# Performance work log

Measured on AMD Instinct MI355X. Metric: run time of the kernel, lower is better.

## Reference

```python
import jax, jax.numpy as jnp
import numpy as np

N_CLASSES = 256
PER_CLASS = 128
N_SUPPORT = 5
N_QUERY = PER_CLASS - N_SUPPORT  # 123
N_VIEW = 2
D = 384
N = N_CLASSES * PER_CLASS  # 32768


def setup_inputs() -> dict:
    key = jax.random.key(0)
    k1, k2 = jax.random.split(key, 2)
    reps = jax.random.normal(k1, (N, N_VIEW, D), dtype=jnp.float32)
    # block-sorted labels: class c occupies rows [c*PER_CLASS, (c+1)*PER_CLASS)
    labels = (jnp.arange(N, dtype=jnp.int32) // PER_CLASS).astype(jnp.int32)
    return {"reps": reps, "labels": labels}


def reference(reps, labels):
    # labels are block-sorted per class, so the original's
    # labels.eq(c).nonzero()[:n_support] / [n_support:] gathers are static reshapes.
    reps_r = reps.reshape(N_CLASSES, PER_CLASS, N_VIEW, D)
    # class-mean prototypes over the support set: [C, V, D]
    prototypes = reps_r[:, :N_SUPPORT].mean(axis=1)
    # query samples: [C*N_QUERY, V, D]
    queries = reps_r[:, N_SUPPORT:].reshape(N_CLASSES * N_QUERY, N_VIEW, D)

    x2 = jnp.sum(queries * queries, axis=-1)            # [n, V]
    y2 = jnp.sum(prototypes * prototypes, axis=-1)      # [m, V]
    xy = jnp.einsum('nvd,mvd->nmv', queries, prototypes)  # [n, m, V]
    dists = x2[:, None, :] + y2[None, :, :] - 2.0 * xy

    # log_softmax over the prototype (class) axis
    log_p_y = jax.nn.log_softmax(-dists, axis=1)
    log_p_y = log_p_y.reshape(N_CLASSES, N_QUERY, N_CLASSES, N_VIEW)

    # gather the true-class log-prob for each query / view
    cls = jnp.arange(N_CLASSES)
    correct = log_p_y[cls, :, cls, :]  # [C, N_QUERY, V]
    loss = -correct.mean()
    return loss
```

## Files before the change

kernel.cpp:

```cpp
#include <hip/hip_runtime.h>
#include <hip/hip_bf16.h>
#include <math.h>

#define NCLS 256
#define PER_CLASS 128
#define NSUP 5
#define NQRY 123
#define NVIEW 2
#define DD 384
#define NQ_TOT (NCLS * NQRY)
#define BM 128
#define BK 32
#define NKT (DD / BK)
#define PS 32
#define NBUF 3

typedef __attribute__((ext_vector_type(8))) short short8;
typedef __attribute__((ext_vector_type(4))) float floatx4;

union FragU { uint4 u; short8 s; };
union PkU { __hip_bfloat162 b2; unsigned int u; };

__device__ __forceinline__ unsigned int cvt2bf(float lo, float hi) {
    PkU p;
    p.b2 = __float22bfloat162_rn(make_float2(lo, hi));
    return p.u;
}

__device__ __forceinline__ void gll16(const ushort* g, ushort* l) {
    __builtin_amdgcn_global_load_lds(
        (const __attribute__((address_space(1))) unsigned int*)g,
        (__attribute__((address_space(3))) unsigned int*)l, 16, 0, 0);
}

#define BARRIER() asm volatile("s_waitcnt lgkmcnt(0)\n\ts_barrier" ::: "memory")
#define WAITVM(n) asm volatile("s_waitcnt vmcnt(" #n ")" ::: "memory")

__global__ __launch_bounds__(384) void proto_kernel(const float* __restrict__ reps,
                                                    ushort* __restrict__ pbf,
                                                    float* __restrict__ y2,
                                                    float* __restrict__ out) {
    __shared__ float wp[6];
    const int b = blockIdx.x;
    const int c = b & 255, v = b >> 8;
    const int d = threadIdx.x;
    if (b == 0 && d == 0) out[0] = 0.f;
    const float* p = reps + ((size_t)(c * PER_CLASS) * NVIEW + v) * DD + d;
    float s = 0.f;
#pragma unroll
    for (int k = 0; k < NSUP; ++k) s += p[(size_t)k * NVIEW * DD];
    s *= 0.2f;
    __hip_bfloat16 h = __float2bfloat16(s);
    pbf[(size_t)b * DD + d] = *reinterpret_cast<ushort*>(&h);
    float q = s * s;
#pragma unroll
    for (int o = 1; o < 64; o <<= 1) q += __shfl_xor(q, o);
    if ((d & 63) == 0) wp[d >> 6] = q;
    __syncthreads();
    if (d == 0) y2[b] = wp[0] + wp[1] + wp[2] + wp[3] + wp[4] + wp[5];
}

__global__ __launch_bounds__(256, 2) void main_kernel(const float* __restrict__ reps,
                                                      const ushort* __restrict__ pbf,
                                                      const float* __restrict__ y2g,
                                                      float* __restrict__ out) {
    __shared__ ushort p_lds[NBUF][NCLS * PS];
    __shared__ float pmx[BM][2];
    __shared__ float pse[BM][2];
    __shared__ float wred[8];

    const int t = threadIdx.x;
    const int v = blockIdx.y;
    const int q0 = blockIdx.x * BM;
    const int wave = t >> 6;
    const int lane = t & 63;
    const int col = lane & 15;
    const int quad = lane >> 4;
    const int wm = wave >> 1;
    const int wn = wave & 1;

    const ushort* psrc = pbf + (size_t)(v * NCLS + wave * 64 + (lane >> 2)) * DD
                             + (((lane & 3) ^ ((lane >> 3) & 3)) << 3);

    const int sP = (col >> 1) & 3;
    const int pbase = (wn * 128 + col) * PS + ((quad ^ sP) << 3);

    const float* qb[4];
#pragma unroll
    for (int mt = 0; mt < 4; ++mt) {
        const int nq = q0 + wm * 64 + mt * 16 + col;
        qb[mt] = reps +
            (size_t)((nq / NQRY) * PER_CLASS + NSUP + (nq % NQRY)) * (NVIEW * DD) +
            v * DD + quad * 8;
    }

    floatx4 acc[4][8];
#pragma unroll
    for (int mt = 0; mt < 4; ++mt)
#pragma unroll
        for (int nt = 0; nt < 8; ++nt) acc[mt][nt] = (floatx4)0.f;

    float4 qv[4][2];

#define LOADQ(kt)                                                                  \
    do {                                                                           \
        _Pragma("unroll") for (int mt = 0; mt < 4; ++mt) {                         \
            qv[mt][0] = *(const float4*)(qb[mt] + (kt) * BK);                      \
            qv[mt][1] = *(const float4*)(qb[mt] + (kt) * BK + 4);                  \
        }                                                                          \
    } while (0)

#define GLLP(kt, b)                                                                \
    do {                                                                           \
        _Pragma("unroll") for (int i = 0; i < 4; ++i)                              \
            gll16(psrc + i * (16 * DD) + (kt) * BK,                                \
                  &p_lds[b][wave * 2048 + i * 512]);                               \
    } while (0)

#define COMPUTE(b)                                                                 \
    do {                                                                           \
        short8 af[4];                                                              \
        _Pragma("unroll") for (int mt = 0; mt < 4; ++mt) {                         \
            FragU f;                                                               \
            f.u.x = cvt2bf(qv[mt][0].x, qv[mt][0].y);                              \
            f.u.y = cvt2bf(qv[mt][0].z, qv[mt][0].w);                              \
            f.u.z = cvt2bf(qv[mt][1].x, qv[mt][1].y);                              \
            f.u.w = cvt2bf(qv[mt][1].z, qv[mt][1].w);                              \
            af[mt] = f.s;                                                          \
        }                                                                          \
        _Pragma("unroll") for (int nt = 0; nt < 8; ++nt) {                         \
            FragU bb;                                                              \
            bb.u = *(const uint4*)&p_lds[b][pbase + nt * 16 * PS];                 \
            _Pragma("unroll") for (int mt = 0; mt < 4; ++mt)                       \
                acc[mt][nt] = __builtin_amdgcn_mfma_f32_16x16x32_bf16(af[mt], bb.s, acc[mt][nt], 0, 0, 0); \
        }                                                                          \
    } while (0)

    GLLP(0, 0);
    GLLP(1, 1);
    WAITVM(4);
    BARRIER();

#pragma unroll
    for (int kt = 0; kt < NKT; ++kt) {
        if (kt < NKT - 2) GLLP(kt + 2, (kt + 2) % NBUF);
        LOADQ(kt);
        if (kt < NKT - 2) {
            WAITVM(12);
        } else {
            WAITVM(0);
        }
        COMPUTE(kt % NBUF);
        if (kt < NKT - 1) BARRIER();
    }

    float y2c[8];
#pragma unroll
    for (int nt = 0; nt < 8; ++nt) y2c[nt] = y2g[v * NCLS + wn * 128 + nt * 16 + col];

    float corr = 0.f;
#pragma unroll
    for (int mt = 0; mt < 4; ++mt) {
#pragma unroll
        for (int r = 0; r < 4; ++r) {
            const int qloc = wm * 64 + mt * 16 + quad * 4 + r;
            const int n = q0 + qloc;
            const int cn = n / NQRY;
            float s[8];
            float mx = -1e30f;
#pragma unroll
            for (int nt = 0; nt < 8; ++nt) {
                s[nt] = 2.f * acc[mt][nt][r] - y2c[nt];
                mx = fmaxf(mx, s[nt]);
                if (cn == wn * 128 + nt * 16 + col) corr += s[nt];
            }
#pragma unroll
            for (int o = 1; o < 16; o <<= 1) mx = fmaxf(mx, __shfl_xor(mx, o));
            float e = 0.f;
#pragma unroll
            for (int nt = 0; nt < 8; ++nt) e += __expf(s[nt] - mx);
#pragma unroll
            for (int o = 1; o < 16; o <<= 1) e += __shfl_xor(e, o);
            if (col == 0) { pmx[qloc][wn] = mx; pse[qloc][wn] = e; }
        }
    }
#pragma unroll
    for (int o = 1; o < 64; o <<= 1) corr += __shfl_xor(corr, o);
    if (lane == 0) wred[wave] = corr;
    __syncthreads();

    float lval = 0.f;
    if (t < BM) {
        float m0 = pmx[t][0], m1 = pmx[t][1];
        float M = fmaxf(m0, m1);
        float E = pse[t][0] * __expf(m0 - M) + pse[t][1] * __expf(m1 - M);
        lval = M + __logf(E);
    }
#pragma unroll
    for (int o = 1; o < 64; o <<= 1) lval += __shfl_xor(lval, o);
    if (lane == 0) wred[4 + wave] = lval;
    __syncthreads();

    if (t == 0) {
        float tot = (wred[4] + wred[5] + wred[6] + wred[7]) -
                    (wred[0] + wred[1] + wred[2] + wred[3]);
        atomicAdd(out, tot * (1.f / (float)(NQ_TOT * NVIEW)));
    }
}

extern "C" void kernel_launch(void* const* d_in, const int* in_sizes, int n_in,
                              void* d_out, int out_size, void* d_ws, size_t ws_size,
                              hipStream_t stream) {
    const float* reps = (const float*)d_in[0];
    float* ws = (float*)d_ws;
    ushort* pbf = (ushort*)ws;
    float* y2 = (float*)(pbf + NVIEW * NCLS * DD);
    float* out = (float*)d_out;

    proto_kernel<<<dim3(NVIEW * NCLS), dim3(DD), 0, stream>>>(reps, pbf, y2, out);
    main_kernel<<<dim3(NQ_TOT / BM, NVIEW), dim3(256), 0, stream>>>(reps, pbf, y2, out);
}
```

Before: 174.3 us.

## Split class axis across blocks with resident prototype LDS and combine kernel

Partitions the 256 prototypes into four 64-class slices handled by separate blocks, each loading its whole bf16 prototype slice into LDS once and streaming queries through a three-deep register prefetch ring. Per-slice partial max and sum-exp are written to global memory and a new combine kernel performs the final log-sum-exp and reduction. This removes per-k-step barriers and LDS buffer rotation and increases block count, but each query row is now read four times from global memory and an extra launch plus intermediate traffic is added.

```diff
diff --git a/kernel.cpp b/kernel.cpp
--- a/kernel.cpp
+++ b/kernel.cpp
@@ -9,11 +9,11 @@
 #define NVIEW 2
 #define DD 384
 #define NQ_TOT (NCLS * NQRY)
-#define BM 128
+#define QB 256
+#define CQ 64
 #define BK 32
 #define NKT (DD / BK)
-#define PS 32
-#define NBUF 3
+#define INV_CNT (1.f / (float)(NQ_TOT * NVIEW))
 
 typedef __attribute__((ext_vector_type(8))) short short8;
 typedef __attribute__((ext_vector_type(4))) float floatx4;
@@ -39,12 +39,13 @@
 __global__ __launch_bounds__(384) void proto_kernel(const float* __restrict__ reps,
                                                     ushort* __restrict__ pbf,
                                                     float* __restrict__ y2,
+                                                    float* __restrict__ wsc,
                                                     float* __restrict__ out) {
     __shared__ float wp[6];
     const int b = blockIdx.x;
     const int c = b & 255, v = b >> 8;
     const int d = threadIdx.x;
-    if (b == 0 && d == 0) out[0] = 0.f;
+    if (b == 0 && d == 0) { out[0] = 0.f; wsc[0] = 0.f; }
     const float* p = reps + ((size_t)(c * PER_CLASS) * NVIEW + v) * DD + d;
     float s = 0.f;
 #pragma unroll
@@ -60,151 +61,165 @@
     if (d == 0) y2[b] = wp[0] + wp[1] + wp[2] + wp[3] + wp[4] + wp[5];
 }
 
-__global__ __launch_bounds__(256, 2) void main_kernel(const float* __restrict__ reps,
-                                                      const ushort* __restrict__ pbf,
-                                                      const float* __restrict__ y2g,
-                                                      float* __restrict__ out) {
-    __shared__ ushort p_lds[NBUF][NCLS * PS];
-    __shared__ float pmx[BM][2];
-    __shared__ float pse[BM][2];
-    __shared__ float wred[8];
+__global__ __launch_bounds__(512) void main_kernel(const float* __restrict__ reps,
+                                                   const ushort* __restrict__ pbf,
+                                                   const float* __restrict__ y2g,
+                                                   float* __restrict__ pmax_g,
+                                                   float* __restrict__ pse_g,
+                                                   float* __restrict__ wsc) {
+    __shared__ ushort p_lds[NKT * CQ * 32];
 
     const int t = threadIdx.x;
     const int v = blockIdx.y;
-    const int q0 = blockIdx.x * BM;
+    const int zq = blockIdx.z;
+    const int q0 = blockIdx.x * QB;
     const int wave = t >> 6;
     const int lane = t & 63;
     const int col = lane & 15;
     const int quad = lane >> 4;
-    const int wm = wave >> 1;
-    const int wn = wave & 1;
-
-    const ushort* psrc = pbf + (size_t)(v * NCLS + wave * 64 + (lane >> 2)) * DD
-                             + (((lane & 3) ^ ((lane >> 3) & 3)) << 3);
-
-    const int sP = (col >> 1) & 3;
-    const int pbase = (wn * 128 + col) * PS + ((quad ^ sP) << 3);
-
-    const float* qb[4];
-#pragma unroll
-    for (int mt = 0; mt < 4; ++mt) {
-        const int nq = q0 + wm * 64 + mt * 16 + col;
+
+#pragma unroll
+    for (int i = 0; i < 6; ++i) {
+        const int g = wave * 6 + i;
+        const int slab = g >> 2;
+        const int sub = g & 3;
+        const ushort* src = pbf +
+            (size_t)(v * NCLS + zq * CQ + sub * 16 + (lane >> 2)) * DD +
+            slab * BK + (lane & 3) * 8;
+        gll16(src, &p_lds[slab * 2048 + sub * 512]);
+    }
+
+    const float* qb[2];
+#pragma unroll
+    for (int mt = 0; mt < 2; ++mt) {
+        const int nq = q0 + wave * 32 + mt * 16 + col;
         qb[mt] = reps +
             (size_t)((nq / NQRY) * PER_CLASS + NSUP + (nq % NQRY)) * (NVIEW * DD) +
             v * DD + quad * 8;
     }
 
-    floatx4 acc[4][8];
-#pragma unroll
-    for (int mt = 0; mt < 4; ++mt)
-#pragma unroll
-        for (int nt = 0; nt < 8; ++nt) acc[mt][nt] = (floatx4)0.f;
-
-    float4 qv[4][2];
-
-#define LOADQ(kt)                                                                  \
+    floatx4 acc[2][4];
+#pragma unroll
+    for (int mt = 0; mt < 2; ++mt)
+#pragma unroll
+        for (int nt = 0; nt < 4; ++nt) acc[mt][nt] = (floatx4)0.f;
+
+    float4 qv[3][2][2];
+
+#define LOADQ(kt, b)                                                               \
     do {                                                                           \
-        _Pragma("unroll") for (int mt = 0; mt < 4; ++mt) {                         \
-            qv[mt][0] = *(const float4*)(qb[mt] + (kt) * BK);                      \
-            qv[mt][1] = *(const float4*)(qb[mt] + (kt) * BK + 4);                  \
+        _Pragma("unroll") for (int mt = 0; mt < 2; ++mt) {                         \
+            qv[b][mt][0] = *(const float4*)(qb[mt] + (kt) * BK);                   \
+            qv[b][mt][1] = *(const float4*)(qb[mt] + (kt) * BK + 4);               \
         }                                                                          \
     } while (0)
 
-#define GLLP(kt, b)                                                                \
-    do {                                                                           \
-        _Pragma("unroll") for (int i = 0; i < 4; ++i)                              \
-            gll16(psrc + i * (16 * DD) + (kt) * BK,                                \
-                  &p_lds[b][wave * 2048 + i * 512]);                               \
-    } while (0)
-
-#define COMPUTE(b)                                                                 \
-    do {                                                                           \
-        short8 af[4];                                                              \
-        _Pragma("unroll") for (int mt = 0; mt < 4; ++mt) {                         \
-            FragU f;                                                               \
-            f.u.x = cvt2bf(qv[mt][0].x, qv[mt][0].y);                              \
-            f.u.y = cvt2bf(qv[mt][0].z, qv[mt][0].w);                              \
-            f.u.z = cvt2bf(qv[mt][1].x, qv[mt][1].y);                              \
-            f.u.w = cvt2bf(qv[mt][1].z, qv[mt][1].w);                              \
-            af[mt] = f.s;                                                          \
-        }                                                                          \
-        _Pragma("unroll") for (int nt = 0; nt < 8; ++nt) {                         \
-            FragU bb;                                                              \
-            bb.u = *(const uint4*)&p_lds[b][pbase + nt * 16 * PS];                 \
-            _Pragma("unroll") for (int mt = 0; mt < 4; ++mt)                       \
-                acc[mt][nt] = __builtin_amdgcn_mfma_f32_16x16x32_bf16(af[mt], bb.s, acc[mt][nt], 0, 0, 0); \
-        }                                                                          \
-    } while (0)
-
-    GLLP(0, 0);
-    GLLP(1, 1);
-    WAITVM(4);
+    LOADQ(0, 0);
+    LOADQ(1, 1);
+    WAITVM(0);
     BARRIER();
 
 #pragma unroll
     for (int kt = 0; kt < NKT; ++kt) {
-        if (kt < NKT - 2) GLLP(kt + 2, (kt + 2) % NBUF);
-        LOADQ(kt);
-        if (kt < NKT - 2) {
-            WAITVM(12);
-        } else {
-            WAITVM(0);
+        if (kt + 2 < NKT) LOADQ(kt + 2, (kt + 2) % 3);
+        short8 af[2];
+#pragma unroll
+        for (int mt = 0; mt < 2; ++mt) {
+            FragU f;
+            f.u.x = cvt2bf(qv[kt % 3][mt][0].x, qv[kt % 3][mt][0].y);
+            f.u.y = cvt2bf(qv[kt % 3][mt][0].z, qv[kt % 3][mt][0].w);
+            f.u.z = cvt2bf(qv[kt % 3][mt][1].x, qv[kt % 3][mt][1].y);
+            f.u.w = cvt2bf(qv[kt % 3][mt][1].z, qv[kt % 3][mt][1].w);
+            af[mt] = f.s;
         }
-        COMPUTE(kt % NBUF);
-        if (kt < NKT - 1) BARRIER();
-    }
-
-    float y2c[8];
-#pragma unroll
-    for (int nt = 0; nt < 8; ++nt) y2c[nt] = y2g[v * NCLS + wn * 128 + nt * 16 + col];
+#pragma unroll
+        for (int nt = 0; nt < 4; ++nt) {
+            FragU bb;
+            bb.u = *(const uint4*)&p_lds[kt * 2048 + (nt * 16 + col) * 32 + quad * 8];
+#pragma unroll
+            for (int mt = 0; mt < 2; ++mt)
+                acc[mt][nt] = __builtin_amdgcn_mfma_f32_16x16x32_bf16(af[mt], bb.s, acc[mt][nt], 0, 0, 0);
+        }
+    }
+
+    float y2c[4];
+#pragma unroll
+    for (int nt = 0; nt < 4; ++nt) y2c[nt] = y2g[v * NCLS + zq * CQ + nt * 16 + col];
 
     float corr = 0.f;
 #pragma unroll
-    for (int mt = 0; mt < 4; ++mt) {
+    for (int mt = 0; mt < 2; ++mt) {
 #pragma unroll
         for (int r = 0; r < 4; ++r) {
-            const int qloc = wm * 64 + mt * 16 + quad * 4 + r;
-            const int n = q0 + qloc;
+            const int n = q0 + wave * 32 + mt * 16 + quad * 4 + r;
             const int cn = n / NQRY;
-            float s[8];
+            float s[4];
             float mx = -1e30f;
 #pragma unroll
-            for (int nt = 0; nt < 8; ++nt) {
+            for (int nt = 0; nt < 4; ++nt) {
                 s[nt] = 2.f * acc[mt][nt][r] - y2c[nt];
                 mx = fmaxf(mx, s[nt]);
-                if (cn == wn * 128 + nt * 16 + col) corr += s[nt];
+                if (cn == zq * CQ + nt * 16 + col) corr += s[nt];
             }
 #pragma unroll
             for (int o = 1; o < 16; o <<= 1) mx = fmaxf(mx, __shfl_xor(mx, o));
             float e = 0.f;
 #pragma unroll
-            for (int nt = 0; nt < 8; ++nt) e += __expf(s[nt] - mx);
+            for (int nt = 0; nt < 4; ++nt) e += __expf(s[nt] - mx);
 #pragma unroll
             for (int o = 1; o < 16; o <<= 1) e += __shfl_xor(e, o);
-            if (col == 0) { pmx[qloc][wn] = mx; pse[qloc][wn] = e; }
+            if (col == 0) {
+                const size_t idx = (size_t)(v * 4 + zq) * NQ_TOT + n;
+                pmax_g[idx] = mx;
+                pse_g[idx] = e;
+            }
         }
     }
 #pragma unroll
     for (int o = 1; o < 64; o <<= 1) corr += __shfl_xor(corr, o);
+
+    __syncthreads();
+    float* wred = (float*)&p_lds[0];
     if (lane == 0) wred[wave] = corr;
     __syncthreads();
-
-    float lval = 0.f;
-    if (t < BM) {
-        float m0 = pmx[t][0], m1 = pmx[t][1];
-        float M = fmaxf(m0, m1);
-        float E = pse[t][0] * __expf(m0 - M) + pse[t][1] * __expf(m1 - M);
-        lval = M + __logf(E);
-    }
+    if (t == 0) {
+        float bc = wred[0] + wred[1] + wred[2] + wred[3] +
+                   wred[4] + wred[5] + wred[6] + wred[7];
+        atomicAdd(wsc, bc);
+    }
+}
+
+__global__ __launch_bounds__(512) void combine_kernel(const float* __restrict__ pmax_g,
+                                                      const float* __restrict__ pse_g,
+                                                      const float* __restrict__ wsc,
+                                                      float* __restrict__ out) {
+    __shared__ float wred[8];
+    const int idx = blockIdx.x * 512 + threadIdx.x;
+    const int v = idx / NQ_TOT;
+    const int n = idx - v * NQ_TOT;
+
+    float m[4], se[4];
+#pragma unroll
+    for (int zq = 0; zq < 4; ++zq) {
+        const size_t i = (size_t)(v * 4 + zq) * NQ_TOT + n;
+        m[zq] = pmax_g[i];
+        se[zq] = pse_g[i];
+    }
+    const float M = fmaxf(fmaxf(m[0], m[1]), fmaxf(m[2], m[3]));
+    const float E = se[0] * __expf(m[0] - M) + se[1] * __expf(m[1] - M) +
+                    se[2] * __expf(m[2] - M) + se[3] * __expf(m[3] - M);
+    float lval = M + __logf(E);
+
 #pragma unroll
     for (int o = 1; o < 64; o <<= 1) lval += __shfl_xor(lval, o);
-    if (lane == 0) wred[4 + wave] = lval;
-    __syncthreads();
-
-    if (t == 0) {
-        float tot = (wred[4] + wred[5] + wred[6] + wred[7]) -
-                    (wred[0] + wred[1] + wred[2] + wred[3]);
-        atomicAdd(out, tot * (1.f / (float)(NQ_TOT * NVIEW)));
+    const int lane = threadIdx.x & 63, wave = threadIdx.x >> 6;
+    if (lane == 0) wred[wave] = lval;
+    __syncthreads();
+    if (threadIdx.x == 0) {
+        float bs = wred[0] + wred[1] + wred[2] + wred[3] +
+                   wred[4] + wred[5] + wred[6] + wred[7];
+        atomicAdd(out, bs * INV_CNT);
+        if (blockIdx.x == 0) atomicAdd(out, -wsc[0] * INV_CNT);
     }
 }
 
@@ -212,11 +227,16 @@
                               void* d_out, int out_size, void* d_ws, size_t ws_size,
                               hipStream_t stream) {
     const float* reps = (const float*)d_in[0];
-    float* ws = (float*)d_ws;
-    ushort* pbf = (ushort*)ws;
+    ushort* pbf = (ushort*)d_ws;
     float* y2 = (float*)(pbf + NVIEW * NCLS * DD);
+    float* pmax_g = y2 + NVIEW * NCLS;
+    float* pse_g = pmax_g + (size_t)NVIEW * 4 * NQ_TOT;
+    float* wsc = pse_g + (size_t)NVIEW * 4 * NQ_TOT;
     float* out = (float*)d_out;
 
-    proto_kernel<<<dim3(NVIEW * NCLS), dim3(DD), 0, stream>>>(reps, pbf, y2, out);
-    main_kernel<<<dim3(NQ_TOT / BM, NVIEW), dim3(256), 0, stream>>>(reps, pbf, y2, out);
-}
+    proto_kernel<<<dim3(NVIEW * NCLS), dim3(DD), 0, stream>>>(reps, pbf, y2, wsc, out);
+    main_kernel<<<dim3(NQ_TOT / QB, NVIEW, 4), dim3(512), 0, stream>>>(reps, pbf, y2,
+                                                                       pmax_g, pse_g, wsc);
+    combine_kernel<<<dim3(NVIEW * NQ_TOT / 512), dim3(512), 0, stream>>>(pmax_g, pse_g,
+                                                                         wsc, out);
+}
```

New measurement: 196.9 us. 13.0% more time.
